# Optimization experiments

Measured on AMD Instinct MI355X. Metric: run time of the kernel, lower is better.

The kernel has to match this reference:

```python
import jax, jax.numpy as jnp
import numpy as np

TOP_K = 2
ROUTED_SCALE = 1.0


def setup_inputs() -> dict:
    key = jax.random.key(0)
    ks = jax.random.split(key, 8)
    B, S, H, I, E, NS = 2, 1024, 768, 3072, 8, 2
    w = lambda k, shape: jax.random.normal(k, shape, jnp.float32) * 0.02
    return {
        "hidden_states": jax.random.normal(ks[0], (B, S, H), jnp.float32),
        "gate_w": w(ks[1], (E, H)),            # router gate: Linear(H->E, no bias), weight [out,in]
        "shared_gate": w(ks[2], (NS, I, H)),   # stacked shared-expert gate_proj weights
        "shared_up": w(ks[3], (NS, I, H)),
        "shared_down": w(ks[4], (NS, H, I)),
        "routed_gate": w(ks[5], (E, I, H)),    # stacked routed-expert weights
        "routed_up": w(ks[6], (E, I, H)),
        "routed_down": w(ks[7], (E, H, I)),
    }


def _swiglu_all(x, gw, uw, dw):
    """Run all stacked SwiGLU experts on all tokens.
    x: [T,H]; gw,uw: [E,I,H]; dw: [E,H,I] -> [T,E,H]"""
    g = jnp.einsum('th,eih->tei', x, gw)
    u = jnp.einsum('th,eih->tei', x, uw)
    h = jax.nn.silu(g) * u
    return jnp.einsum('tei,ehi->teh', h, dw)


def reference(hidden_states, gate_w, shared_gate, shared_up, shared_down,
              routed_gate, routed_up, routed_down):
    B, S, H = hidden_states.shape
    T = B * S
    x = hidden_states.reshape(T, H)

    # ---- Router (token choice, softmax scoring, no capacity/bias) ----
    router_logits = x @ gate_w.T                      # [T, E]
    scores = jax.nn.softmax(router_logits, axis=-1)   # [T, E]
    _, topk_idx = jax.lax.top_k(scores, TOP_K)        # [T, k]
    topk_w = jnp.take_along_axis(scores, topk_idx, axis=-1)
    topk_w = topk_w / (topk_w.sum(axis=-1, keepdims=True) + 1e-8)
    topk_w = topk_w * ROUTED_SCALE                    # [T, k]

    # Combine matrix: weight for each (token, expert); 0 if not selected.
    E = gate_w.shape[0]
    combine = jnp.zeros((T, E), scores.dtype).at[
        jnp.arange(T)[:, None], topk_idx].add(topk_w)  # [T, E]

    # ---- Routed experts (dense-all-experts, masked combine == dispatch) ----
    routed_all = _swiglu_all(x, routed_gate, routed_up, routed_down)  # [T,E,H]
    routed_out = jnp.einsum('teh,te->th', routed_all, combine)        # [T, H]

    # ---- Shared experts: sum over shared experts / N_shared ----
    NS = shared_gate.shape[0]
    shared_all = _swiglu_all(x, shared_gate, shared_up, shared_down)  # [T,NS,H]
    shared_out = shared_all.sum(axis=1) / NS                          # [T, H]

    out = (shared_out + routed_out).reshape(B, S, H)
    return out
```

## Files before the change

kernel.cpp:

```cpp
#include <hip/hip_runtime.h>
#include <stdint.h>

typedef __attribute__((ext_vector_type(8))) short short8;
typedef __attribute__((ext_vector_type(4))) float f32x4;
typedef __attribute__((ext_vector_type(4))) unsigned short usvec4;

static constexpr int T_ = 2048;
static constexpr int H_ = 768;
static constexpr int I_ = 3072;
static constexpr int RCAP = 6144;
static constexpr int RT_ = RCAP + 2 * T_;
static constexpr int TILE_ = 128;
static constexpr int BK_ = 32;

static constexpr long WE_SG = 0;
static constexpr long WE_SU = 4718592;
static constexpr long WE_SD = 9437184;
static constexpr long WE_RG = 14155776;
static constexpr long WE_RU = 33030144;
static constexpr long WE_RD = 51904512;
static constexpr long OFF_XP   = 141557760;
static constexpr long OFF_HACT = 157286400;
static constexpr long OFF_PART = 220200960;
static constexpr long OFF_META = 245366784;
static constexpr long OFF_TIDX = 245367040;
static constexpr long OFF_TW   = 245383424;
static constexpr long OFF_TOK  = 245399808;
static constexpr long OFF_SLOT = 245440768;
static constexpr long OFF_WL   = 245481728;

__device__ __forceinline__ unsigned short f2bf(float f) {
  union { float f; unsigned u; } v; v.f = f;
  unsigned r = (v.u + 0x7FFFu + ((v.u >> 16) & 1u)) >> 16;
  return (unsigned short)r;
}

__device__ __forceinline__ void gload_lds16(const void* g, void* l) {
  typedef const __attribute__((address_space(1))) void gvoid;
  typedef __attribute__((address_space(3))) void lvoid;
  gvoid* gp = (gvoid*)(uintptr_t)g;
  lvoid* lp = (lvoid*)(uint32_t)(uintptr_t)l;
  __builtin_amdgcn_global_load_lds(gp, lp, 16, 0, 0);
}

__device__ __forceinline__ f32x4 mfma16(short8 a, short8 b, f32x4 c) {
  return __builtin_amdgcn_mfma_f32_16x16x32_bf16(a, b, c, 0, 0, 0);
}

__device__ __forceinline__ short8 ds_read_b128_asm(unsigned int addr) {
  short8 v;
  asm volatile("ds_read_b128 %0, %1" : "=v"(v) : "v"(addr));
  return v;
}

__device__ __forceinline__ void wait_lgkm0_fence() {
  asm volatile("s_waitcnt lgkmcnt(0)" ::: "memory");
  __builtin_amdgcn_sched_barrier(0);
}
__device__ __forceinline__ void wait_vmcnt_barrier6(bool counted) {
  if (counted) asm volatile("s_waitcnt vmcnt(6)" ::: "memory");
  else         asm volatile("s_waitcnt vmcnt(0)" ::: "memory");
  __builtin_amdgcn_s_barrier();
  __builtin_amdgcn_sched_barrier(0);
}
__device__ __forceinline__ void wait_vmcnt_barrier4(bool counted) {
  if (counted) asm volatile("s_waitcnt vmcnt(4)" ::: "memory");
  else         asm volatile("s_waitcnt vmcnt(0)" ::: "memory");
  __builtin_amdgcn_s_barrier();
  __builtin_amdgcn_sched_barrier(0);
}

__device__ __forceinline__ unsigned swz(unsigned o) {
  return o ^ (((o >> 6) & 3u) << 4);
}

__global__ void cast_weights_k(const float* __restrict__ sg, const float* __restrict__ su,
                               const float* __restrict__ sd, const float* __restrict__ rg,
                               const float* __restrict__ ru, const float* __restrict__ rd,
                               unsigned short* __restrict__ wb) {
  long c = (long)blockIdx.x * 256 + threadIdx.x;
  const float* src; long dstoff, lc; int dtype = 0;
  if      (c <  1179648) { src = sg; dstoff = WE_SG; lc = c; }
  else if (c <  2359296) { src = su; dstoff = WE_SU; lc = c - 1179648; }
  else if (c <  3538944) { src = sd; dstoff = WE_SD; lc = c - 2359296; dtype = 1; }
  else if (c <  8257536) { src = rg; dstoff = WE_RG; lc = c - 3538944; }
  else if (c < 12976128) { src = ru; dstoff = WE_RU; lc = c - 8257536; }
  else                   { src = rd; dstoff = WE_RD; lc = c - 12976128; dtype = 1; }
  f32x4 a = ((const f32x4*)src)[lc];
  usvec4 o;
  #pragma unroll
  for (int j = 0; j < 4; j++) o[j] = f2bf(a[j]);
  constexpr long EW = (long)I_ * H_;
  long f = lc * 4;
  long e = f / EW; f -= e * EW;
  long dst;
  if (dtype == 0) {
    int i = (int)(f / H_), h = (int)(f - (long)i * H_);
    dst = dstoff + e * EW + ((long)((i >> 7) * 24 + (h >> 5))) * 4096 + ((i & 127) << 5) + (h & 31);
  } else {
    int h = (int)(f / I_), i = (int)(f - (long)h * I_);
    dst = dstoff + e * EW + ((long)((h >> 7) * 96 + (i >> 5))) * 4096 + ((h & 127) << 5) + (i & 31);
  }
  *(usvec4*)(wb + dst) = o;
}

__global__ void router_k(const float* __restrict__ x, const float* __restrict__ gw,
                         int* __restrict__ tidx, float* __restrict__ tw) {
  const int lane = threadIdx.x & 63;
  const int wv = threadIdx.x >> 6;
  const int t = blockIdx.x * 4 + wv;
  float xv[12];
  #pragma unroll
  for (int j = 0; j < 12; j++) xv[j] = x[(long)t * H_ + lane + j * 64];
  float lg[8];
  #pragma unroll
  for (int e = 0; e < 8; e++) {
    float s = 0.f;
    #pragma unroll
    for (int j = 0; j < 12; j++) s += xv[j] * gw[e * H_ + lane + j * 64];
    #pragma unroll
    for (int o = 32; o > 0; o >>= 1) s += __shfl_xor(s, o, 64);
    lg[e] = s;
  }
  if (lane == 0) {
    float m = lg[0];
    #pragma unroll
    for (int e = 1; e < 8; e++) m = fmaxf(m, lg[e]);
    float ex[8]; float S = 0.f;
    #pragma unroll
    for (int e = 0; e < 8; e++) { ex[e] = __expf(lg[e] - m); S += ex[e]; }
    int i0 = 0;
    #pragma unroll
    for (int e = 1; e < 8; e++) if (ex[e] > ex[i0]) i0 = e;
    int i1 = (i0 == 0) ? 1 : 0;
    #pragma unroll
    for (int e = 0; e < 8; e++) if (e != i0 && ex[e] > ex[i1]) i1 = e;
    float s0 = ex[i0] / S, s1 = ex[i1] / S;
    float den = s0 + s1 + 1e-8f;
    tidx[t * 2] = i0; tidx[t * 2 + 1] = i1;
    tw[t * 2] = s0 / den; tw[t * 2 + 1] = s1 / den;
  }
}

__global__ void pack_k(const int* __restrict__ tidx, const float* __restrict__ tw,
                       int* __restrict__ meta, int* __restrict__ tokL,
                       int* __restrict__ slotL, float* __restrict__ wL) {
  __shared__ int cnt[8], base_s[8], cur[8];
  const int tid = threadIdx.x;
  if (tid < 8) { cnt[tid] = 0; cur[tid] = 0; }
  for (int r = tid; r < RT_; r += 1024) tokL[r] = -1;
  __syncthreads();
  for (int t = tid; t < T_; t += 1024) {
    atomicAdd(&cnt[tidx[t * 2]], 1);
    atomicAdd(&cnt[tidx[t * 2 + 1]], 1);
  }
  __syncthreads();
  if (tid == 0) {
    int run = 0;
    for (int e = 0; e < 8; e++) {
      base_s[e] = run;
      int pad = (cnt[e] + 127) & ~127;
      meta[e] = run;
      meta[10 + e] = pad;
      run += pad;
    }
    for (int s = 0; s < 2; s++) { meta[8 + s] = RCAP + s * T_; meta[18 + s] = T_; }
  }
  __syncthreads();
  for (int t = tid; t < T_; t += 1024) {
    for (int k = 0; k < 2; k++) {
      int e = tidx[t * 2 + k];
      int p = atomicAdd(&cur[e], 1);
      int R = base_s[e] + p;
      tokL[R] = t; slotL[R] = k; wL[R] = tw[t * 2 + k];
    }
    for (int s = 0; s < 2; s++) {
      int R = RCAP + s * T_ + t;
      tokL[R] = t; slotL[R] = 2 + s; wL[R] = 0.5f;
    }
  }
}

__global__ void gather_k(const float* __restrict__ x, const int* __restrict__ tokL,
                         unsigned short* __restrict__ xp) {
  const int r = blockIdx.x, tid = threadIdx.x;
  const int tok = tokL[r];
  const int c = tid * 4;
  usvec4 o = 0;
  if (tok >= 0) {
    f32x4 v = *(const f32x4*)(x + (long)tok * H_ + c);
    #pragma unroll
    for (int j = 0; j < 4; j++) o[j] = f2bf(v[j]);
  }
  long dst = ((long)(r >> 7) * 24 + (c >> 5)) * 4096 + ((r & 127) << 5) + (c & 31);
  *(usvec4*)(xp + dst) = o;
}

__global__ __launch_bounds__(256, 2)
void gemm1_k(const unsigned short* __restrict__ xp,
             const unsigned short* __restrict__ wb,
             const int* __restrict__ meta,
             unsigned short* __restrict__ hact) {
  const int fid = blockIdx.x;
  const int x   = fid & 7;
  const int q   = fid >> 3;
  const int bx  = q & 15;
  const int g   = (q >> 4) * 8 + x;
  const int e   = g / 24;
  const int by  = g % 24;

  const int rowsP = meta[10 + e];
  if (bx * TILE_ >= rowsP) return;
  const int base = meta[e];
  const int n0 = by * TILE_;

  const unsigned short* gwp;
  const unsigned short* uwp;
  if (e < 8) { gwp = wb + WE_RG + (long)e * I_ * H_;       uwp = wb + WE_RU + (long)e * I_ * H_; }
  else       { gwp = wb + WE_SG + (long)(e - 8) * I_ * H_; uwp = wb + WE_SU + (long)(e - 8) * I_ * H_; }

  const int rblk = (base >> 7) + bx;
  const char* aT = (const char*)(xp + (long)rblk * 24 * 4096);
  const char* gT = (const char*)(gwp + (long)by * 24 * 4096);
  const char* uT = (const char*)(uwp + (long)by * 24 * 4096);

  __shared__ alignas(16) unsigned short As[3 * TILE_ * BK_];
  __shared__ alignas(16) unsigned short Bg[3 * TILE_ * BK_];
  __shared__ alignas(16) unsigned short Bu[3 * TILE_ * BK_];

  const int tid = threadIdx.x;
  const unsigned o1 = tid * 16, o2 = 4096 + tid * 16;
  const unsigned s1 = swz(o1), s2 = swz(o2);

  const int lane = tid & 63, wv = tid >> 6;
  const int wm = wv >> 1, wn = wv & 1;
  const int lm = lane & 15, ld = lane >> 4;

  int aOff[4], bOff[4];
  #pragma unroll
  for (int i = 0; i < 4; i++) {
    int ra = wm * 64 + i * 16 + lm;
    int rb = wn * 64 + i * 16 + lm;
    aOff[i] = ra * 64 + ((ld * 16) ^ ((ra & 3) << 4));
    bOff[i] = rb * 64 + ((ld * 16) ^ ((rb & 3) << 4));
  }
  const unsigned asBase = (unsigned)(uintptr_t)As;
  const unsigned bgBase = (unsigned)(uintptr_t)Bg;
  const unsigned buBase = (unsigned)(uintptr_t)Bu;

  f32x4 accG[4][4] = {};
  f32x4 accU[4][4] = {};

  auto stage = [&](int buf, int kk) {
    const long ko = (long)kk * 8192;
    const unsigned bo = buf * 8192;
    gload_lds16(aT + ko + s1, (char*)As + bo + o1);
    gload_lds16(aT + ko + s2, (char*)As + bo + o2);
    gload_lds16(gT + ko + s1, (char*)Bg + bo + o1);
    gload_lds16(gT + ko + s2, (char*)Bg + bo + o2);
    gload_lds16(uT + ko + s1, (char*)Bu + bo + o1);
    gload_lds16(uT + ko + s2, (char*)Bu + bo + o2);
  };

  constexpr int NK = H_ / BK_;
  stage(0, 0);
  stage(1, 1);
  asm volatile("s_waitcnt vmcnt(6)" ::: "memory");
  __builtin_amdgcn_s_barrier();
  __builtin_amdgcn_sched_barrier(0);

  for (int kk = 0; kk < NK; ++kk) {
    const int cur = kk % 3;
    const bool more = (kk + 2 < NK);
    if (more) stage((kk + 2) % 3, kk + 2);
    const unsigned bo = cur * 8192;
    short8 av[4], gv[4], uv[4];
    #pragma unroll
    for (int i = 0; i < 4; i++) {
      av[i] = ds_read_b128_asm(asBase + bo + aOff[i]);
      gv[i] = ds_read_b128_asm(bgBase + bo + bOff[i]);
      uv[i] = ds_read_b128_asm(buBase + bo + bOff[i]);
    }
    wait_lgkm0_fence();
    #pragma unroll
    for (int mi = 0; mi < 4; mi++)
      #pragma unroll
      for (int ni = 0; ni < 4; ni++) {
        accG[mi][ni] = mfma16(av[mi], gv[ni], accG[mi][ni]);
        accU[mi][ni] = mfma16(av[mi], uv[ni], accU[mi][ni]);
      }
    wait_vmcnt_barrier6(more);
  }

  unsigned short* ep = (wv < 2) ? (As + wv * 2048) : (Bg + (wv - 2) * 2048);
  #pragma unroll
  for (int half = 0; half < 2; half++) {
    #pragma unroll
    for (int mi2 = 0; mi2 < 2; mi2++) {
      int mi = half * 2 + mi2;
      #pragma unroll
      for (int ni = 0; ni < 4; ni++) {
        f32x4 g2 = accG[mi][ni], u = accU[mi][ni];
        #pragma unroll
        for (int j = 0; j < 4; j++) {
          float gvv = g2[j];
          float hv = gvv / (1.0f + __expf(-gvv)) * u[j];
          ep[(mi2 * 16 + ld * 4 + j) * 64 + ni * 16 + lm] = f2bf(hv);
        }
      }
    }
    __syncthreads();
    #pragma unroll
    for (int it = 0; it < 4; it++) {
      int r = it * 8 + (lane >> 3);
      int c8 = (lane & 7) * 8;
      short8 v = *(const short8*)(ep + r * 64 + c8);
      int R7 = wm * 64 + half * 32 + r;
      int C = n0 + wn * 64 + c8;
      long dst = ((long)rblk * 96 + (C >> 5)) * 4096 + (R7 << 5) + (C & 31);
      *(short8*)(hact + dst) = v;
    }
    __syncthreads();
  }
}

__global__ __launch_bounds__(256, 3)
void gemm2_k(const unsigned short* __restrict__ hact,
             const unsigned short* __restrict__ wb,
             const int* __restrict__ meta,
             const int* __restrict__ tokL,
             const int* __restrict__ slotL,
             const float* __restrict__ wLst,
             float* __restrict__ parts) {
  const int fid = blockIdx.x;
  const int x   = fid & 7;
  const int q   = fid >> 3;
  const int bx  = q & 15;
  const int g   = (q >> 4) * 8 + x;
  if (g >= 60) return;
  const int e   = g / 6;
  const int by  = g % 6;

  const int rowsP = meta[10 + e];
  if (bx * TILE_ >= rowsP) return;
  const int base = meta[e];
  const int n0 = by * TILE_;
  const unsigned short* dwp = (e < 8) ? wb + WE_RD + (long)e * H_ * I_
                                      : wb + WE_SD + (long)(e - 8) * H_ * I_;
  const int rblk = (base >> 7) + bx;
  const char* aT = (const char*)(hact + (long)rblk * 96 * 4096);
  const char* bT = (const char*)(dwp + (long)by * 96 * 4096);

  __shared__ alignas(16) unsigned short As[3 * TILE_ * BK_];
  __shared__ alignas(16) unsigned short Bd[3 * TILE_ * BK_];
  const int tid = threadIdx.x;
  const unsigned o1 = tid * 16, o2 = 4096 + tid * 16;
  const unsigned s1 = swz(o1), s2 = swz(o2);
  const int lane = tid & 63, wv = tid >> 6;
  const int wm = wv >> 1, wn = wv & 1;
  const int lm = lane & 15, ld = lane >> 4;
  int aOff[4], bOff[4];
  #pragma unroll
  for (int i = 0; i < 4; i++) {
    int ra = wm * 64 + i * 16 + lm;
    int rb = wn * 64 + i * 16 + lm;
    aOff[i] = ra * 64 + ((ld * 16) ^ ((ra & 3) << 4));
    bOff[i] = rb * 64 + ((ld * 16) ^ ((rb & 3) << 4));
  }
  const unsigned asBase = (unsigned)(uintptr_t)As;
  const unsigned bdBase = (unsigned)(uintptr_t)Bd;
  f32x4 acc[4][4] = {};

  auto stage = [&](int buf, int kk) {
    const long ko = (long)kk * 8192;
    const unsigned bo = buf * 8192;
    gload_lds16(aT + ko + s1, (char*)As + bo + o1);
    gload_lds16(aT + ko + s2, (char*)As + bo + o2);
    gload_lds16(bT + ko + s1, (char*)Bd + bo + o1);
    gload_lds16(bT + ko + s2, (char*)Bd + bo + o2);
  };

  constexpr int NK = I_ / BK_;
  stage(0, 0);
  stage(1, 1);
  asm volatile("s_waitcnt vmcnt(4)" ::: "memory");
  __builtin_amdgcn_s_barrier();
  __builtin_amdgcn_sched_barrier(0);

  for (int kk = 0; kk < NK; ++kk) {
    const int cur = kk % 3;
    const bool more = (kk + 2 < NK);
    if (more) stage((kk + 2) % 3, kk + 2);
    const unsigned bo = cur * 8192;
    short8 av[4], bv[4];
    #pragma unroll
    for (int i = 0; i < 4; i++) {
      av[i] = ds_read_b128_asm(asBase + bo + aOff[i]);
      bv[i] = ds_read_b128_asm(bdBase + bo + bOff[i]);
    }
    wait_lgkm0_fence();
    #pragma unroll
    for (int mi = 0; mi < 4; mi++)
      #pragma unroll
      for (int ni = 0; ni < 4; ni++)
        acc[mi][ni] = mfma16(av[mi], bv[ni], acc[mi][ni]);
    wait_vmcnt_barrier4(more);
  }

  const long R0 = base + bx * TILE_ + wm * 64;
  #pragma unroll
  for (int mi = 0; mi < 4; mi++) {
    #pragma unroll
    for (int j = 0; j < 4; j++) {
      long R = R0 + mi * 16 + ld * 4 + j;
      int tok = tokL[R];
      if (tok < 0) continue;
      float w = wLst[R];
      long obase = (long)slotL[R] * (T_ * H_) + (long)tok * H_ + n0 + wn * 64 + lm;
      #pragma unroll
      for (int ni = 0; ni < 4; ni++) {
        parts[obase + ni * 16] = w * acc[mi][ni][j];
      }
    }
  }
}

__global__ void final_k(const float* __restrict__ parts, float* __restrict__ out) {
  const int i = blockIdx.x * 256 + threadIdx.x;
  const int N4 = T_ * H_ / 4;
  const f32x4* p = (const f32x4*)parts;
  f32x4 s = p[i];
  s += p[N4 + i];
  s += p[2 * N4 + i];
  s += p[3 * N4 + i];
  ((f32x4*)out)[i] = s;
}

extern "C" void kernel_launch(void* const* d_in, const int* in_sizes, int n_in,
                              void* d_out, int out_size, void* d_ws, size_t ws_size,
                              hipStream_t stream) {
  (void)in_sizes; (void)n_in; (void)out_size; (void)ws_size;
  const float* x  = (const float*)d_in[0];
  const float* gw = (const float*)d_in[1];
  const float* sg = (const float*)d_in[2];
  const float* su = (const float*)d_in[3];
  const float* sd = (const float*)d_in[4];
  const float* rg = (const float*)d_in[5];
  const float* ru = (const float*)d_in[6];
  const float* rd = (const float*)d_in[7];

  char* ws = (char*)d_ws;
  unsigned short* wb   = (unsigned short*)ws;
  unsigned short* xp   = (unsigned short*)(ws + OFF_XP);
  unsigned short* ha   = (unsigned short*)(ws + OFF_HACT);
  float*          prt  = (float*)(ws + OFF_PART);
  int*            meta = (int*)(ws + OFF_META);
  int*            tidx = (int*)(ws + OFF_TIDX);
  float*          tw   = (float*)(ws + OFF_TW);
  int*            tokL = (int*)(ws + OFF_TOK);
  int*            slotL= (int*)(ws + OFF_SLOT);
  float*          wl   = (float*)(ws + OFF_WL);

  cast_weights_k<<<69120, 256, 0, stream>>>(sg, su, sd, rg, ru, rd, wb);
  router_k<<<512, 256, 0, stream>>>(x, gw, tidx, tw);
  pack_k<<<1, 1024, 0, stream>>>(tidx, tw, meta, tokL, slotL, wl);
  gather_k<<<RT_, 192, 0, stream>>>(x, tokL, xp);
  gemm1_k<<<3840, 256, 0, stream>>>(xp, wb, meta, ha);
  gemm2_k<<<1024, 256, 0, stream>>>(ha, wb, meta, tokL, slotL, wl, prt);
  final_k<<<1536, 256, 0, stream>>>(prt, (float*)d_out);
}
```

Measured before the change: 282.5 us.

## Fuse fp32-to-bf16 weight conversion into GEMM loaders, drop cast kernel

Removes the separate cast_weights_k pass, which read all fp32 expert weights and wrote a tiled bf16 copy. The two GEMM kernels now load fp32 weight rows straight into registers, convert them with v_cvt_pk_bf16_f32, and store them into swizzled LDS inside the pipelined k-loop. The activation tiles still use direct global-to-LDS DMA. This saves one full write and read of the weights, but each GEMM tile now re-reads fp32 weights (twice the bytes) and spends VALU and LDS-store work in the main loop, with more vmcnt/lgkmcnt waits.

```diff
diff --git a/kernel.cpp b/kernel.cpp
--- a/kernel.cpp
+++ b/kernel.cpp
@@ -3,6 +3,7 @@
 
 typedef __attribute__((ext_vector_type(8))) short short8;
 typedef __attribute__((ext_vector_type(4))) float f32x4;
+typedef __attribute__((ext_vector_type(4))) int i32x4;
 typedef __attribute__((ext_vector_type(4))) unsigned short usvec4;
 
 static constexpr int T_ = 2048;
@@ -10,15 +11,8 @@
 static constexpr int I_ = 3072;
 static constexpr int RCAP = 6144;
 static constexpr int RT_ = RCAP + 2 * T_;
-static constexpr int TILE_ = 128;
 static constexpr int BK_ = 32;
 
-static constexpr long WE_SG = 0;
-static constexpr long WE_SU = 4718592;
-static constexpr long WE_SD = 9437184;
-static constexpr long WE_RG = 14155776;
-static constexpr long WE_RU = 33030144;
-static constexpr long WE_RD = 51904512;
 static constexpr long OFF_XP   = 141557760;
 static constexpr long OFF_HACT = 157286400;
 static constexpr long OFF_PART = 220200960;
@@ -57,51 +51,21 @@
   asm volatile("s_waitcnt lgkmcnt(0)" ::: "memory");
   __builtin_amdgcn_sched_barrier(0);
 }
-__device__ __forceinline__ void wait_vmcnt_barrier6(bool counted) {
-  if (counted) asm volatile("s_waitcnt vmcnt(6)" ::: "memory");
-  else         asm volatile("s_waitcnt vmcnt(0)" ::: "memory");
-  __builtin_amdgcn_s_barrier();
-  __builtin_amdgcn_sched_barrier(0);
-}
-__device__ __forceinline__ void wait_vmcnt_barrier4(bool counted) {
-  if (counted) asm volatile("s_waitcnt vmcnt(4)" ::: "memory");
-  else         asm volatile("s_waitcnt vmcnt(0)" ::: "memory");
-  __builtin_amdgcn_s_barrier();
-  __builtin_amdgcn_sched_barrier(0);
+
+__device__ __forceinline__ int cvtpk(float a, float b) {
+  unsigned r;
+  asm("v_cvt_pk_bf16_f32 %0, %1, %2" : "=v"(r) : "v"(a), "v"(b));
+  return (int)r;
+}
+__device__ __forceinline__ i32x4 pk4(f32x4 a, f32x4 b) {
+  i32x4 r;
+  r[0] = cvtpk(a[0], a[1]); r[1] = cvtpk(a[2], a[3]);
+  r[2] = cvtpk(b[0], b[1]); r[3] = cvtpk(b[2], b[3]);
+  return r;
 }
 
 __device__ __forceinline__ unsigned swz(unsigned o) {
   return o ^ (((o >> 6) & 3u) << 4);
-}
-
-__global__ void cast_weights_k(const float* __restrict__ sg, const float* __restrict__ su,
-                               const float* __restrict__ sd, const float* __restrict__ rg,
-                               const float* __restrict__ ru, const float* __restrict__ rd,
-                               unsigned short* __restrict__ wb) {
-  long c = (long)blockIdx.x * 256 + threadIdx.x;
-  const float* src; long dstoff, lc; int dtype = 0;
-  if      (c <  1179648) { src = sg; dstoff = WE_SG; lc = c; }
-  else if (c <  2359296) { src = su; dstoff = WE_SU; lc = c - 1179648; }
-  else if (c <  3538944) { src = sd; dstoff = WE_SD; lc = c - 2359296; dtype = 1; }
-  else if (c <  8257536) { src = rg; dstoff = WE_RG; lc = c - 3538944; }
-  else if (c < 12976128) { src = ru; dstoff = WE_RU; lc = c - 8257536; }
-  else                   { src = rd; dstoff = WE_RD; lc = c - 12976128; dtype = 1; }
-  f32x4 a = ((const f32x4*)src)[lc];
-  usvec4 o;
-  #pragma unroll
-  for (int j = 0; j < 4; j++) o[j] = f2bf(a[j]);
-  constexpr long EW = (long)I_ * H_;
-  long f = lc * 4;
-  long e = f / EW; f -= e * EW;
-  long dst;
-  if (dtype == 0) {
-    int i = (int)(f / H_), h = (int)(f - (long)i * H_);
-    dst = dstoff + e * EW + ((long)((i >> 7) * 24 + (h >> 5))) * 4096 + ((i & 127) << 5) + (h & 31);
-  } else {
-    int h = (int)(f / I_), i = (int)(f - (long)h * I_);
-    dst = dstoff + e * EW + ((long)((h >> 7) * 96 + (i >> 5))) * 4096 + ((h & 127) << 5) + (i & 31);
-  }
-  *(usvec4*)(wb + dst) = o;
 }
 
 __global__ void router_k(const float* __restrict__ x, const float* __restrict__ gw,
@@ -198,44 +162,47 @@
 
 __global__ __launch_bounds__(256, 2)
 void gemm1_k(const unsigned short* __restrict__ xp,
-             const unsigned short* __restrict__ wb,
+             const float* __restrict__ rg, const float* __restrict__ ru,
+             const float* __restrict__ sgw, const float* __restrict__ suw,
              const int* __restrict__ meta,
              unsigned short* __restrict__ hact) {
   const int fid = blockIdx.x;
-  const int x   = fid & 7;
+  const int xc  = fid & 7;
   const int q   = fid >> 3;
   const int bx  = q & 15;
-  const int g   = (q >> 4) * 8 + x;
+  const int g   = (q >> 4) * 8 + xc;
   const int e   = g / 24;
   const int by  = g % 24;
 
   const int rowsP = meta[10 + e];
-  if (bx * TILE_ >= rowsP) return;
+  if (bx * 128 >= rowsP) return;
   const int base = meta[e];
-  const int n0 = by * TILE_;
-
-  const unsigned short* gwp;
-  const unsigned short* uwp;
-  if (e < 8) { gwp = wb + WE_RG + (long)e * I_ * H_;       uwp = wb + WE_RU + (long)e * I_ * H_; }
-  else       { gwp = wb + WE_SG + (long)(e - 8) * I_ * H_; uwp = wb + WE_SU + (long)(e - 8) * I_ * H_; }
+  const int n0 = by * 128;
+
+  const float* gw32; const float* uw32;
+  if (e < 8) { gw32 = rg + (long)e * I_ * H_;        uw32 = ru + (long)e * I_ * H_; }
+  else       { gw32 = sgw + (long)(e - 8) * I_ * H_; uw32 = suw + (long)(e - 8) * I_ * H_; }
 
   const int rblk = (base >> 7) + bx;
   const char* aT = (const char*)(xp + (long)rblk * 24 * 4096);
-  const char* gT = (const char*)(gwp + (long)by * 24 * 4096);
-  const char* uT = (const char*)(uwp + (long)by * 24 * 4096);
-
-  __shared__ alignas(16) unsigned short As[3 * TILE_ * BK_];
-  __shared__ alignas(16) unsigned short Bg[3 * TILE_ * BK_];
-  __shared__ alignas(16) unsigned short Bu[3 * TILE_ * BK_];
+
+  __shared__ alignas(16) unsigned short As[3 * 4096];
+  __shared__ alignas(16) unsigned short Bg[3 * 4096];
+  __shared__ alignas(16) unsigned short Bu[3 * 4096];
 
   const int tid = threadIdx.x;
   const unsigned o1 = tid * 16, o2 = 4096 + tid * 16;
   const unsigned s1 = swz(o1), s2 = swz(o2);
 
+  const int wr = tid >> 1, wh = tid & 1;
+  const float* gRow = gw32 + (long)(n0 + wr) * H_ + wh * 16;
+  const float* uRow = uw32 + (long)(n0 + wr) * H_ + wh * 16;
+  const unsigned wo0 = (unsigned)(wr * 64 + wh * 32);
+  const unsigned wd0 = swz(wo0), wd1 = swz(wo0 + 16);
+
   const int lane = tid & 63, wv = tid >> 6;
   const int wm = wv >> 1, wn = wv & 1;
   const int lm = lane & 15, ld = lane >> 4;
-
   int aOff[4], bOff[4];
   #pragma unroll
   for (int i = 0; i < 4; i++) {
@@ -250,30 +217,31 @@
 
   f32x4 accG[4][4] = {};
   f32x4 accU[4][4] = {};
-
-  auto stage = [&](int buf, int kk) {
+  f32x4 gS[4], uS[4];
+
+  auto ADMA = [&](int kk) {
     const long ko = (long)kk * 8192;
-    const unsigned bo = buf * 8192;
+    const unsigned bo = (unsigned)((kk % 3) * 8192);
     gload_lds16(aT + ko + s1, (char*)As + bo + o1);
     gload_lds16(aT + ko + s2, (char*)As + bo + o2);
-    gload_lds16(gT + ko + s1, (char*)Bg + bo + o1);
-    gload_lds16(gT + ko + s2, (char*)Bg + bo + o2);
-    gload_lds16(uT + ko + s1, (char*)Bu + bo + o1);
-    gload_lds16(uT + ko + s2, (char*)Bu + bo + o2);
-  };
-
-  constexpr int NK = H_ / BK_;
-  stage(0, 0);
-  stage(1, 1);
-  asm volatile("s_waitcnt vmcnt(6)" ::: "memory");
-  __builtin_amdgcn_s_barrier();
-  __builtin_amdgcn_sched_barrier(0);
-
-  for (int kk = 0; kk < NK; ++kk) {
-    const int cur = kk % 3;
-    const bool more = (kk + 2 < NK);
-    if (more) stage((kk + 2) % 3, kk + 2);
-    const unsigned bo = cur * 8192;
+  };
+  auto LOADW = [&](int kk) {
+    const float* gp = gRow + kk * 32;
+    const float* up = uRow + kk * 32;
+    #pragma unroll
+    for (int j = 0; j < 4; j++) gS[j] = *(const f32x4*)(gp + j * 4);
+    #pragma unroll
+    for (int j = 0; j < 4; j++) uS[j] = *(const f32x4*)(up + j * 4);
+  };
+  auto CVTW = [&](int kk) {
+    const unsigned bo = (unsigned)((kk % 3) * 8192);
+    *(i32x4*)((char*)Bg + bo + wd0) = pk4(gS[0], gS[1]);
+    *(i32x4*)((char*)Bg + bo + wd1) = pk4(gS[2], gS[3]);
+    *(i32x4*)((char*)Bu + bo + wd0) = pk4(uS[0], uS[1]);
+    *(i32x4*)((char*)Bu + bo + wd1) = pk4(uS[2], uS[3]);
+  };
+  auto COMP = [&](int kk) {
+    const unsigned bo = (unsigned)((kk % 3) * 8192);
     short8 av[4], gv[4], uv[4];
     #pragma unroll
     for (int i = 0; i < 4; i++) {
@@ -289,7 +257,33 @@
         accG[mi][ni] = mfma16(av[mi], gv[ni], accG[mi][ni]);
         accU[mi][ni] = mfma16(av[mi], uv[ni], accU[mi][ni]);
       }
-    wait_vmcnt_barrier6(more);
+  };
+
+  constexpr int NK = H_ / BK_;
+  ADMA(0); LOADW(0);
+  asm volatile("s_waitcnt vmcnt(0)" ::: "memory");
+  CVTW(0);
+  ADMA(1); LOADW(1);
+  asm volatile("s_waitcnt lgkmcnt(0)" ::: "memory");
+  __builtin_amdgcn_s_barrier();
+  __builtin_amdgcn_sched_barrier(0);
+
+  for (int k = 0; k < NK; ++k) {
+    if (k + 2 < NK) ADMA(k + 2);
+    __builtin_amdgcn_sched_barrier(0);
+    COMP(k);
+    if (k + 1 < NK) {
+      if (k + 2 < NK) asm volatile("s_waitcnt vmcnt(2)" ::: "memory");
+      else            asm volatile("s_waitcnt vmcnt(0)" ::: "memory");
+      CVTW(k + 1);
+      if (k + 2 < NK) LOADW(k + 2);
+      asm volatile("s_waitcnt lgkmcnt(0)" ::: "memory");
+      __builtin_amdgcn_s_barrier();
+      __builtin_amdgcn_sched_barrier(0);
+    } else {
+      __builtin_amdgcn_s_barrier();
+      __builtin_amdgcn_sched_barrier(0);
+    }
   }
 
   unsigned short* ep = (wv < 2) ? (As + wv * 2048) : (Bg + (wv - 2) * 2048);
@@ -326,36 +320,41 @@
 
 __global__ __launch_bounds__(256, 3)
 void gemm2_k(const unsigned short* __restrict__ hact,
-             const unsigned short* __restrict__ wb,
+             const float* __restrict__ rd, const float* __restrict__ sd,
              const int* __restrict__ meta,
              const int* __restrict__ tokL,
              const int* __restrict__ slotL,
              const float* __restrict__ wLst,
              float* __restrict__ parts) {
   const int fid = blockIdx.x;
-  const int x   = fid & 7;
+  const int xc  = fid & 7;
   const int q   = fid >> 3;
   const int bx  = q & 15;
-  const int g   = (q >> 4) * 8 + x;
+  const int g   = (q >> 4) * 8 + xc;
   if (g >= 60) return;
   const int e   = g / 6;
   const int by  = g % 6;
 
   const int rowsP = meta[10 + e];
-  if (bx * TILE_ >= rowsP) return;
+  if (bx * 128 >= rowsP) return;
   const int base = meta[e];
-  const int n0 = by * TILE_;
-  const unsigned short* dwp = (e < 8) ? wb + WE_RD + (long)e * H_ * I_
-                                      : wb + WE_SD + (long)(e - 8) * H_ * I_;
+  const int n0 = by * 128;
+  const float* dw32 = (e < 8) ? rd + (long)e * H_ * I_
+                              : sd + (long)(e - 8) * H_ * I_;
   const int rblk = (base >> 7) + bx;
   const char* aT = (const char*)(hact + (long)rblk * 96 * 4096);
-  const char* bT = (const char*)(dwp + (long)by * 96 * 4096);
-
-  __shared__ alignas(16) unsigned short As[3 * TILE_ * BK_];
-  __shared__ alignas(16) unsigned short Bd[3 * TILE_ * BK_];
+
+  __shared__ alignas(16) unsigned short As[3 * 4096];
+  __shared__ alignas(16) unsigned short Bd[3 * 4096];
   const int tid = threadIdx.x;
   const unsigned o1 = tid * 16, o2 = 4096 + tid * 16;
   const unsigned s1 = swz(o1), s2 = swz(o2);
+
+  const int wr = tid >> 1, wh = tid & 1;
+  const float* dRow = dw32 + (long)(n0 + wr) * I_ + wh * 16;
+  const unsigned wo0 = (unsigned)(wr * 64 + wh * 32);
+  const unsigned wd0 = swz(wo0), wd1 = swz(wo0 + 16);
+
   const int lane = tid & 63, wv = tid >> 6;
   const int wm = wv >> 1, wn = wv & 1;
   const int lm = lane & 15, ld = lane >> 4;
@@ -370,28 +369,26 @@
   const unsigned asBase = (unsigned)(uintptr_t)As;
   const unsigned bdBase = (unsigned)(uintptr_t)Bd;
   f32x4 acc[4][4] = {};
-
-  auto stage = [&](int buf, int kk) {
+  f32x4 dS[4];
+
+  auto ADMA = [&](int kk) {
     const long ko = (long)kk * 8192;
-    const unsigned bo = buf * 8192;
+    const unsigned bo = (unsigned)((kk % 3) * 8192);
     gload_lds16(aT + ko + s1, (char*)As + bo + o1);
     gload_lds16(aT + ko + s2, (char*)As + bo + o2);
-    gload_lds16(bT + ko + s1, (char*)Bd + bo + o1);
-    gload_lds16(bT + ko + s2, (char*)Bd + bo + o2);
-  };
-
-  constexpr int NK = I_ / BK_;
-  stage(0, 0);
-  stage(1, 1);
-  asm volatile("s_waitcnt vmcnt(4)" ::: "memory");
-  __builtin_amdgcn_s_barrier();
-  __builtin_amdgcn_sched_barrier(0);
-
-  for (int kk = 0; kk < NK; ++kk) {
-    const int cur = kk % 3;
-    const bool more = (kk + 2 < NK);
-    if (more) stage((kk + 2) % 3, kk + 2);
-    const unsigned bo = cur * 8192;
+  };
+  auto LOADW = [&](int kk) {
+    const float* dp = dRow + kk * 32;
+    #pragma unroll
+    for (int j = 0; j < 4; j++) dS[j] = *(const f32x4*)(dp + j * 4);
+  };
+  auto CVTW = [&](int kk) {
+    const unsigned bo = (unsigned)((kk % 3) * 8192);
+    *(i32x4*)((char*)Bd + bo + wd0) = pk4(dS[0], dS[1]);
+    *(i32x4*)((char*)Bd + bo + wd1) = pk4(dS[2], dS[3]);
+  };
+  auto COMP = [&](int kk) {
+    const unsigned bo = (unsigned)((kk % 3) * 8192);
     short8 av[4], bv[4];
     #pragma unroll
     for (int i = 0; i < 4; i++) {
@@ -404,10 +401,36 @@
       #pragma unroll
       for (int ni = 0; ni < 4; ni++)
         acc[mi][ni] = mfma16(av[mi], bv[ni], acc[mi][ni]);
-    wait_vmcnt_barrier4(more);
-  }
-
-  const long R0 = base + bx * TILE_ + wm * 64;
+  };
+
+  constexpr int NK = I_ / BK_;
+  ADMA(0); LOADW(0);
+  asm volatile("s_waitcnt vmcnt(0)" ::: "memory");
+  CVTW(0);
+  ADMA(1); LOADW(1);
+  asm volatile("s_waitcnt lgkmcnt(0)" ::: "memory");
+  __builtin_amdgcn_s_barrier();
+  __builtin_amdgcn_sched_barrier(0);
+
+  for (int k = 0; k < NK; ++k) {
+    if (k + 2 < NK) ADMA(k + 2);
+    __builtin_amdgcn_sched_barrier(0);
+    COMP(k);
+    if (k + 1 < NK) {
+      if (k + 2 < NK) asm volatile("s_waitcnt vmcnt(2)" ::: "memory");
+      else            asm volatile("s_waitcnt vmcnt(0)" ::: "memory");
+      CVTW(k + 1);
+      if (k + 2 < NK) LOADW(k + 2);
+      asm volatile("s_waitcnt lgkmcnt(0)" ::: "memory");
+      __builtin_amdgcn_s_barrier();
+      __builtin_amdgcn_sched_barrier(0);
+    } else {
+      __builtin_amdgcn_s_barrier();
+      __builtin_amdgcn_sched_barrier(0);
+    }
+  }
+
+  const long R0 = base + bx * 128 + wm * 64;
   #pragma unroll
   for (int mi = 0; mi < 4; mi++) {
     #pragma unroll
@@ -450,7 +473,6 @@
   const float* rd = (const float*)d_in[7];
 
   char* ws = (char*)d_ws;
-  unsigned short* wb   = (unsigned short*)ws;
   unsigned short* xp   = (unsigned short*)(ws + OFF_XP);
   unsigned short* ha   = (unsigned short*)(ws + OFF_HACT);
   float*          prt  = (float*)(ws + OFF_PART);
@@ -461,11 +483,10 @@
   int*            slotL= (int*)(ws + OFF_SLOT);
   float*          wl   = (float*)(ws + OFF_WL);
 
-  cast_weights_k<<<69120, 256, 0, stream>>>(sg, su, sd, rg, ru, rd, wb);
   router_k<<<512, 256, 0, stream>>>(x, gw, tidx, tw);
   pack_k<<<1, 1024, 0, stream>>>(tidx, tw, meta, tokL, slotL, wl);
   gather_k<<<RT_, 192, 0, stream>>>(x, tokL, xp);
-  gemm1_k<<<3840, 256, 0, stream>>>(xp, wb, meta, ha);
-  gemm2_k<<<1024, 256, 0, stream>>>(ha, wb, meta, tokL, slotL, wl, prt);
+  gemm1_k<<<3840, 256, 0, stream>>>(xp, rg, ru, sg, su, meta, ha);
+  gemm2_k<<<1024, 256, 0, stream>>>(ha, rd, sd, meta, tokL, slotL, wl, prt);
   final_k<<<1536, 256, 0, stream>>>(prt, (float*)d_out);
 }
```

Result: slower. 342.7 us (+21.3%).
